# Performance work log

Measured on AMD Instinct MI355X. Metric: run time of the kernel, lower is better.

## Reference

```python
import jax, jax.numpy as jnp
import numpy as np

M, B, U, D = 65536, 128, 256, 512
USAGE_DECAY = 0.95

def _l2n(x, axis):
    # tf.nn.l2_normalize semantics (K.l2_normalize)
    return x / jnp.sqrt(jnp.maximum(jnp.sum(x * x, axis=axis, keepdims=True), 1e-12))

def _lstm_cell(x, h, c, kernel, rec_kernel, bias):
    # Keras LSTMCell: gates in order i, f, c, o
    z = x @ kernel + h @ rec_kernel + bias  # [B, 4U]
    zi, zf, zc, zo = jnp.split(z, 4, axis=-1)
    i = jax.nn.sigmoid(zi)
    f = jax.nn.sigmoid(zf)
    c_new = f * c + i * jnp.tanh(zc)
    o = jax.nn.sigmoid(zo)
    h_new = o * jnp.tanh(c_new)
    return h_new, c_new

def setup_inputs() -> dict:
    key = jax.random.key(0)
    ks = jax.random.split(key, 10)
    return {
        "inputs": jax.random.normal(ks[0], (B, D), jnp.float32),
        "r_tm1": jnp.zeros((B, U), jnp.float32),
        "m_tm1": jax.random.uniform(ks[1], (M, U), jnp.float32),
        "c_wu_tm1": jax.random.uniform(ks[2], (M, B), jnp.float32),
        "c_wlu_tm1": jnp.zeros((M, B), jnp.float32),
        "c_wr_tm1": jax.random.uniform(ks[3], (M, B), jnp.float32),
        "h_tm1": jax.random.normal(ks[4], (B, U), jnp.float32) * 0.1,
        "cc_tm1": jax.random.normal(ks[5], (B, U), jnp.float32) * 0.1,
        "kernel": jax.random.normal(ks[6], (D + U, 4 * U), jnp.float32) * 0.02,
        "rec_kernel": jax.random.normal(ks[7], (U, 4 * U), jnp.float32) * 0.02,
        "bias": jnp.zeros((4 * U,), jnp.float32),
        "write_gate": jax.random.normal(ks[8], (1,), jnp.float32),
    }

def reference(inputs, r_tm1, m_tm1, c_wu_tm1, c_wlu_tm1, c_wr_tm1,
              h_tm1, cc_tm1, kernel, rec_kernel, bias, write_gate):
    # Controller step on [inputs, r_tm1]
    ctrl_in = jnp.concatenate([inputs, r_tm1], axis=1)          # [B, D+U]
    key_list, cc = _lstm_cell(ctrl_in, h_tm1, cc_tm1, kernel, rec_kernel, bias)  # [B, U]

    wg = jax.nn.sigmoid(write_gate)                              # [1]
    # NOTE: faithful to source -- scalar (1 - wg) is ADDED elementwise, then c_wlu added
    c_ww = wg * c_wr_tm1 + (1.0 - wg) + c_wlu_tm1                # [M, B]

    # cosine-similarity addressing
    cos = _l2n(key_list, 1) @ _l2n(m_tm1, 1).T                   # [B, M]
    # K.softmax on the transposed matrix => softmax over the BATCH axis (faithful)
    c_wr = jax.nn.softmax(cos.T, axis=-1)                        # [M, B]
    read = c_wr.T @ m_tm1                                        # [B, U]

    c_wu = USAGE_DECAY * c_wu_tm1 + c_wr + c_ww                  # [M, B]

    # top_k(c_wu.T, M): v.T[-1,:] is the per-batch minimum over slots
    mins = jnp.min(c_wu, axis=0)                                 # [B]
    min_idx = jnp.argmin(c_wu, axis=0)                           # [B]
    b_star = jnp.argmin(mins)                                    # scalar
    i_star = min_idx[b_star]                                     # global least-used slot

    c_wlu = (c_wu <= mins[None, :]).astype(jnp.float32)          # [M, B]

    # zeroing_matrix = one_hot(i_star broadcast to B cols, on=0, off=1) [M,B];
    # dot(zeroing[M,B], ones[B,U]) -> rows = B except zeroed row (faithful B scaling)
    keep = 1.0 - jax.nn.one_hot(i_star, M, dtype=jnp.float32)    # [M]
    memory = (float(B) * keep)[:, None] * m_tm1                  # [M, U]
    memory = c_ww @ key_list + memory                            # [M, U]

    return (read, memory, c_wu, c_wlu, c_wr, key_list, cc)
```

## Files before the change

### kernel.cpp

```cpp
#include <hip/hip_runtime.h>
#include <hip/hip_bf16.h>
#include <math.h>

#define NM 65536
#define NB 128
#define NU 256
#define ND 512

constexpr size_t OUT_READ = 0;
constexpr size_t OUT_MEM  = 32768;
constexpr size_t OUT_CWU  = OUT_MEM + 16777216;
constexpr size_t OUT_CWLU = OUT_CWU + 8388608;
constexpr size_t OUT_CWR  = OUT_CWLU + 8388608;
constexpr size_t OUT_KEY  = OUT_CWR + 8388608;
constexpr size_t OUT_CC   = OUT_KEY + 32768;

constexpr size_t WS_KLNT   = 0;
constexpr size_t WS_MINENC = 131072;
constexpr size_t WS_MINS   = 132096;
constexpr size_t WS_ISTAR  = 132608;
constexpr size_t WS_PART   = 135168;

typedef __attribute__((ext_vector_type(8))) short short8v;
typedef __attribute__((ext_vector_type(4))) float floatx4;

__device__ __forceinline__ unsigned fenc(float x) {
    unsigned u = __float_as_uint(x);
    return (u & 0x80000000u) ? ~u : (u | 0x80000000u);
}
__device__ __forceinline__ float fdec(unsigned e) {
    unsigned u = (e & 0x80000000u) ? (e ^ 0x80000000u) : ~e;
    return __uint_as_float(u);
}
__device__ __forceinline__ float sigm(float x) { return 1.0f / (1.0f + expf(-x)); }
__device__ __forceinline__ unsigned short f2b(float f) {
    __hip_bfloat16 h = __float2bfloat16(f);
    return *reinterpret_cast<unsigned short*>(&h);
}

__global__ __launch_bounds__(256) void k_lstm(
    const float* __restrict__ xin_g, const float* __restrict__ r_tm1,
    const float* __restrict__ h_tm1, const float* __restrict__ cc_tm1,
    const float* __restrict__ Wk, const float* __restrict__ Wr,
    const float* __restrict__ bias, float* __restrict__ out,
    float* __restrict__ klnT, unsigned long long* __restrict__ minenc)
{
    const int b = blockIdx.x, t = threadIdx.x;
    __shared__ float xin[ND + NU];
    __shared__ float hh[NU];
    __shared__ float red[NU];
    for (int k = t; k < ND; k += 256) xin[k] = xin_g[b * ND + k];
    xin[ND + t] = r_tm1[b * NU + t];
    hh[t] = h_tm1[b * NU + t];
    out[OUT_READ + b * NU + t] = 0.f;
    if (b == 0 && t < NB) minenc[t] = ~0ULL;
    __syncthreads();

    float zi = bias[t], zf = bias[NU + t], zc = bias[2 * NU + t], zo = bias[3 * NU + t];
    #pragma unroll 4
    for (int k = 0; k < ND + NU; ++k) {
        const float x = xin[k];
        const float* w = Wk + (size_t)k * (4 * NU);
        zi += x * w[t]; zf += x * w[NU + t]; zc += x * w[2 * NU + t]; zo += x * w[3 * NU + t];
    }
    #pragma unroll 4
    for (int k = 0; k < NU; ++k) {
        const float x = hh[k];
        const float* w = Wr + (size_t)k * (4 * NU);
        zi += x * w[t]; zf += x * w[NU + t]; zc += x * w[2 * NU + t]; zo += x * w[3 * NU + t];
    }
    const float gi = sigm(zi), gf = sigm(zf), gc = tanhf(zc), go = sigm(zo);
    const float cold = cc_tm1[b * NU + t];
    const float cn = __fadd_rn(__fmul_rn(gf, cold), __fmul_rn(gi, gc));
    const float hn = __fmul_rn(go, tanhf(cn));
    out[OUT_KEY + b * NU + t] = hn;
    out[OUT_CC + b * NU + t] = cn;
    red[t] = hn * hn;
    __syncthreads();
    for (int s = 128; s > 0; s >>= 1) { if (t < s) red[t] += red[t + s]; __syncthreads(); }
    const float nrm = sqrtf(fmaxf(red[0], 1e-12f));
    klnT[t * NB + b] = hn / nrm;
}

__global__ __launch_bounds__(256, 2) void k_dot(
    const float* __restrict__ mT, const float* __restrict__ klnT,
    const float* __restrict__ cwr_t, const float* __restrict__ cwlu_t,
    const float* __restrict__ cwu_t, const float* __restrict__ wgp,
    float* __restrict__ out, unsigned long long* __restrict__ minenc)
{
    __shared__ float smem[16384];
    __shared__ float rn_s[128];
    const int t = threadIdx.x, w = t >> 6, l = t & 63;
    const int tx = t & 15, ty = t >> 4;
    const int b0 = tx * 8, s0 = ty * 8;
    const int sb = blockIdx.x * 128;

    #pragma unroll 4
    for (int i = 0; i < 32; ++i) {
        const int s = w * 32 + i;
        const float4 mv = *(const float4*)(mT + (size_t)(sb + s) * NU + l * 4);
        float ss = mv.x * mv.x + mv.y * mv.y + mv.z * mv.z + mv.w * mv.w;
        #pragma unroll
        for (int d = 1; d < 64; d <<= 1) ss += __shfl_xor(ss, d);
        if (l == 0) rn_s[s] = sqrtf(fmaxf(ss, 1e-12f));
    }

    const int sl = t & 127, ug = t >> 7;
    const int ku_ = t >> 4, kb = (t & 15) * 4;

    float acc[8][8];
    #pragma unroll
    for (int i = 0; i < 8; ++i)
        #pragma unroll
        for (int j = 0; j < 8; ++j) acc[i][j] = 0.f;

    float4 gm[2], gk[2];
    #pragma unroll
    for (int i = 0; i < 2; ++i) {
        gm[i] = *(const float4*)(mT + (size_t)(sb + sl) * NU + (ug + 2 * i) * 4);
        gk[i] = *(const float4*)(klnT + (size_t)ku_ * NB + kb + i * 64);
    }
    for (int c = 0; c < 16; ++c) {
        const int mo = (c & 1) * 2048;
        const int ko = 4096 + (c & 1) * 2048;
        #pragma unroll
        for (int i = 0; i < 2; ++i) {
            const int uo = (ug + 2 * i) * 4;
            smem[mo + (uo + 0) * 128 + sl] = gm[i].x;
            smem[mo + (uo + 1) * 128 + sl] = gm[i].y;
            smem[mo + (uo + 2) * 128 + sl] = gm[i].z;
            smem[mo + (uo + 3) * 128 + sl] = gm[i].w;
            *(float4*)&smem[ko + ku_ * 128 + kb + i * 64] = gk[i];
        }
        __syncthreads();
        if (c < 15) {
            const int uc = (c + 1) * 16;
            #pragma unroll
            for (int i = 0; i < 2; ++i) {
                gm[i] = *(const float4*)(mT + (size_t)(sb + sl) * NU + uc + (ug + 2 * i) * 4);
                gk[i] = *(const float4*)(klnT + (size_t)(uc + ku_) * NB + kb + i * 64);
            }
        }
        #pragma unroll 4
        for (int u = 0; u < 16; ++u) {
            const float4 sv0 = *(const float4*)&smem[mo + u * 128 + s0];
            const float4 sv1 = *(const float4*)&smem[mo + u * 128 + s0 + 4];
            const float4 kv0 = *(const float4*)&smem[ko + u * 128 + b0];
            const float4 kv1 = *(const float4*)&smem[ko + u * 128 + b0 + 4];
            const float sv[8] = {sv0.x, sv0.y, sv0.z, sv0.w, sv1.x, sv1.y, sv1.z, sv1.w};
            const float kv[8] = {kv0.x, kv0.y, kv0.z, kv0.w, kv1.x, kv1.y, kv1.z, kv1.w};
            #pragma unroll
            for (int i = 0; i < 8; ++i)
                #pragma unroll
                for (int j = 0; j < 8; ++j)
                    acc[i][j] += sv[i] * kv[j];
        }
        __syncthreads();
    }

    #pragma unroll
    for (int i = 0; i < 8; ++i) {
        *(float4*)&smem[(s0 + i) * 128 + b0]     = make_float4(acc[i][0], acc[i][1], acc[i][2], acc[i][3]);
        *(float4*)&smem[(s0 + i) * 128 + b0 + 4] = make_float4(acc[i][4], acc[i][5], acc[i][6], acc[i][7]);
    }
    __syncthreads();

    const float wg = sigm(wgp[0]);
    const float omw = __fsub_rn(1.f, wg);
    unsigned long long lmin0 = ~0ULL, lmin1 = ~0ULL;
    #pragma unroll 2
    for (int i = 0; i < 32; ++i) {
        const int s = w * 32 + i;
        const int m = sb + s;
        const float2 dv = *(const float2*)&smem[s * 128 + 2 * l];
        const float rnv = rn_s[s];
        const float2 wrt = ((const float2*)(cwr_t + (size_t)m * NB))[l];
        const float2 wlu = ((const float2*)(cwlu_t + (size_t)m * NB))[l];
        const float2 wut = ((const float2*)(cwu_t + (size_t)m * NB))[l];
        const float c0 = dv.x / rnv, c1 = dv.y / rnv;
        float mx = fmaxf(c0, c1);
        #pragma unroll
        for (int d = 1; d < 64; d <<= 1) mx = fmaxf(mx, __shfl_xor(mx, d));
        const float e0 = expf(c0 - mx), e1 = expf(c1 - mx);
        float sm = e0 + e1;
        #pragma unroll
        for (int d = 1; d < 64; d <<= 1) sm += __shfl_xor(sm, d);
        const float w0 = e0 / sm, w1 = e1 / sm;
        const float cww0 = __fadd_rn(__fadd_rn(__fmul_rn(wg, wrt.x), omw), wlu.x);
        const float cww1 = __fadd_rn(__fadd_rn(__fmul_rn(wg, wrt.y), omw), wlu.y);
        const float cu0 = __fadd_rn(__fadd_rn(__fmul_rn(0.95f, wut.x), w0), cww0);
        const float cu1 = __fadd_rn(__fadd_rn(__fmul_rn(0.95f, wut.y), w1), cww1);
        ((float2*)(out + OUT_CWR))[(size_t)m * 64 + l] = make_float2(w0, w1);
        ((float2*)(out + OUT_CWU))[(size_t)m * 64 + l] = make_float2(cu0, cu1);
        const unsigned long long e0u = (((unsigned long long)fenc(cu0)) << 32) | (unsigned)m;
        const unsigned long long e1u = (((unsigned long long)fenc(cu1)) << 32) | (unsigned)m;
        lmin0 = (e0u < lmin0) ? e0u : lmin0;
        lmin1 = (e1u < lmin1) ? e1u : lmin1;
    }
    atomicMin(&minenc[2 * l], lmin0);
    atomicMin(&minenc[2 * l + 1], lmin1);
}

__global__ void k_argmin(const unsigned long long* __restrict__ minenc,
                         float* __restrict__ mins, unsigned* __restrict__ istar)
{
    __shared__ unsigned long long red[NB];
    const int t = threadIdx.x;
    const unsigned long long e = minenc[t];
    const unsigned enc32 = (unsigned)(e >> 32);
    mins[t] = fdec(enc32);
    red[t] = (((unsigned long long)enc32) << 32) | (unsigned)t;
    __syncthreads();
    for (int s = 64; s > 0; s >>= 1) {
        if (t < s) { const unsigned long long o = red[t + s]; if (o < red[t]) red[t] = o; }
        __syncthreads();
    }
    if (t == 0) {
        const unsigned bstar = (unsigned)(red[0] & 0xFFFFFFFFu);
        istar[0] = (unsigned)(minenc[bstar] & 0xFFFFFFFFu);
    }
}

__global__ __launch_bounds__(256, 2) void k_mem(
    const float* __restrict__ mT,
    const float* __restrict__ cwr_t, const float* __restrict__ cwlu_t,
    const float* __restrict__ wgp, const float* __restrict__ mins,
    const unsigned* __restrict__ istar_p, float* __restrict__ out)
{
    __shared__ unsigned short cwwb[128 * 136];
    __shared__ unsigned short keyT[128 * 136];
    const int t = threadIdx.x, w = t >> 6, l = t & 63;
    const int sb = blockIdx.x * 128;
    const float wg = sigm(wgp[0]);
    const float omw = __fsub_rn(1.f, wg);
    const int istar = (int)istar_p[0];

    {
        const int srow = t >> 5;
        const int bc = (t & 31) * 4;
        for (int it = 0; it < 16; ++it) {
            const int s = it * 8 + srow;
            const size_t row = (size_t)(sb + s) * NB + bc;
            const float4 wr = *(const float4*)(cwr_t + row);
            const float4 lu = *(const float4*)(cwlu_t + row);
            const float4 wu = *(const float4*)(out + OUT_CWU + row);
            float4 cw;
            cw.x = __fadd_rn(__fadd_rn(__fmul_rn(wg, wr.x), omw), lu.x);
            cw.y = __fadd_rn(__fadd_rn(__fmul_rn(wg, wr.y), omw), lu.y);
            cw.z = __fadd_rn(__fadd_rn(__fmul_rn(wg, wr.z), omw), lu.z);
            cw.w = __fadd_rn(__fadd_rn(__fmul_rn(wg, wr.w), omw), lu.w);
            ushort4 pk;
            pk.x = f2b(cw.x); pk.y = f2b(cw.y); pk.z = f2b(cw.z); pk.w = f2b(cw.w);
            *(ushort4*)&cwwb[s * 136 + bc] = pk;
            const float4 mb = *(const float4*)(mins + bc);
            float4 wl;
            wl.x = (wu.x <= mb.x) ? 1.f : 0.f;
            wl.y = (wu.y <= mb.y) ? 1.f : 0.f;
            wl.z = (wu.z <= mb.z) ? 1.f : 0.f;
            wl.w = (wu.w <= mb.w) ? 1.f : 0.f;
            *(float4*)(out + OUT_CWLU + row) = wl;
        }
    }

    const int rk = (l >> 4) * 8;
    const int rr = l & 15;

    for (int uh = 0; uh < 2; ++uh) {
        if (uh) __syncthreads();
        {
            const int br = t >> 5;
            const int ko = (t & 31) * 4;
            for (int it = 0; it < 16; ++it) {
                const int b = it * 8 + br;
                const float4 kv = *(const float4*)(out + OUT_KEY + (size_t)b * NU + uh * 128 + ko);
                keyT[(ko + 0) * 136 + b] = f2b(kv.x);
                keyT[(ko + 1) * 136 + b] = f2b(kv.y);
                keyT[(ko + 2) * 136 + b] = f2b(kv.z);
                keyT[(ko + 3) * 136 + b] = f2b(kv.w);
            }
        }
        __syncthreads();

        floatx4 acc0[8], acc1[8];
        #pragma unroll
        for (int ut = 0; ut < 8; ++ut) {
            acc0[ut] = (floatx4){0.f, 0.f, 0.f, 0.f};
            acc1[ut] = (floatx4){0.f, 0.f, 0.f, 0.f};
        }
        #pragma unroll
        for (int kc = 0; kc < 4; ++kc) {
            const short8v a0 = *(const short8v*)&cwwb[(w * 32 + rr) * 136 + kc * 32 + rk];
            const short8v a1 = *(const short8v*)&cwwb[(w * 32 + 16 + rr) * 136 + kc * 32 + rk];
            #pragma unroll
            for (int ut = 0; ut < 8; ++ut) {
                const short8v bf = *(const short8v*)&keyT[(ut * 16 + rr) * 136 + kc * 32 + rk];
                acc0[ut] = __builtin_amdgcn_mfma_f32_16x16x32_bf16(a0, bf, acc0[ut], 0, 0, 0);
                acc1[ut] = __builtin_amdgcn_mfma_f32_16x16x32_bf16(a1, bf, acc1[ut], 0, 0, 0);
            }
        }

        #pragma unroll
        for (int ut = 0; ut < 8; ++ut) {
            const int gcol = uh * 128 + ut * 16 + rr;
            #pragma unroll
            for (int q = 0; q < 4; ++q) {
                const int grow0 = sb + w * 32 + (l >> 4) * 4 + q;
                const int grow1 = grow0 + 16;
                const float mv0 = mT[(size_t)grow0 * NU + gcol];
                const float mv1 = mT[(size_t)grow1 * NU + gcol];
                const float kf0 = (grow0 == istar) ? 0.f : 128.f;
                const float kf1 = (grow1 == istar) ? 0.f : 128.f;
                out[OUT_MEM + (size_t)grow0 * NU + gcol] = acc0[ut][q] + kf0 * mv0;
                out[OUT_MEM + (size_t)grow1 * NU + gcol] = acc1[ut][q] + kf1 * mv1;
            }
        }
    }
}

template <int USE_PART>
__global__ __launch_bounds__(256) void k_read(
    const float* __restrict__ mT, float* __restrict__ out, float* __restrict__ part)
{
    __shared__ float m_ch[2][8][128];
    __shared__ float cwr_ch[2][8][128];
    const int t = threadIdx.x;
    const int r = blockIdx.x, ri = r >> 1, uh = r & 1;
    const int s0 = ri * 256;
    const int b0 = (t & 15) * 8, u0 = (t >> 4) * 8;
    const int ssl = t >> 5, sul = (t & 31) * 4;

    float4 acc[8][2];
    #pragma unroll
    for (int bi = 0; bi < 8; ++bi) { acc[bi][0] = make_float4(0,0,0,0); acc[bi][1] = make_float4(0,0,0,0); }

    float4 pm = *(const float4*)(mT + (size_t)(s0 + ssl) * NU + uh * 128 + sul);
    float4 pc = *(const float4*)(out + OUT_CWR + (size_t)(s0 + ssl) * NB + sul);

    for (int c = 0; c < 32; ++c) {
        const int buf = c & 1;
        *(float4*)&m_ch[buf][ssl][sul] = pm;
        *(float4*)&cwr_ch[buf][ssl][sul] = pc;
        __syncthreads();
        if (c + 1 < 32) {
            const size_t sn = (size_t)(s0 + (c + 1) * 8 + ssl);
            pm = *(const float4*)(mT + sn * NU + uh * 128 + sul);
            pc = *(const float4*)(out + OUT_CWR + sn * NB + sul);
        }
        #pragma unroll
        for (int sj = 0; sj < 8; ++sj) {
            const float4 ca = *(const float4*)&cwr_ch[buf][sj][b0];
            const float4 cb = *(const float4*)&cwr_ch[buf][sj][b0 + 4];
            const float4 ma = *(const float4*)&m_ch[buf][sj][u0];
            const float4 mb = *(const float4*)&m_ch[buf][sj][u0 + 4];
            const float cwa[8] = {ca.x, ca.y, ca.z, ca.w, cb.x, cb.y, cb.z, cb.w};
            #pragma unroll
            for (int bi = 0; bi < 8; ++bi) {
                acc[bi][0].x += cwa[bi] * ma.x; acc[bi][0].y += cwa[bi] * ma.y;
                acc[bi][0].z += cwa[bi] * ma.z; acc[bi][0].w += cwa[bi] * ma.w;
                acc[bi][1].x += cwa[bi] * mb.x; acc[bi][1].y += cwa[bi] * mb.y;
                acc[bi][1].z += cwa[bi] * mb.z; acc[bi][1].w += cwa[bi] * mb.w;
            }
        }
    }

    if (USE_PART) {
        float* dst = part + (size_t)r * (128 * 128);
        #pragma unroll
        for (int bi = 0; bi < 8; ++bi) {
            *(float4*)(dst + (size_t)(b0 + bi) * 128 + u0) = acc[bi][0];
            *(float4*)(dst + (size_t)(b0 + bi) * 128 + u0 + 4) = acc[bi][1];
        }
    } else {
        #pragma unroll
        for (int bi = 0; bi < 8; ++bi) {
            const float v[8] = {acc[bi][0].x, acc[bi][0].y, acc[bi][0].z, acc[bi][0].w,
                                acc[bi][1].x, acc[bi][1].y, acc[bi][1].z, acc[bi][1].w};
            #pragma unroll
            for (int q = 0; q < 8; ++q)
                atomicAdd(out + OUT_READ + (size_t)(b0 + bi) * NU + uh * 128 + u0 + q, v[q]);
        }
    }
}

__global__ __launch_bounds__(256) void k_redread(const float* __restrict__ part,
                                                 float* __restrict__ out)
{
    const int b = blockIdx.x, u = threadIdx.x;
    const int uh = u >> 7, ul = u & 127;
    float s = 0.f;
    #pragma unroll 4
    for (int ri = 0; ri < 256; ++ri)
        s += part[((size_t)(ri * 2 + uh) * 128 + b) * 128 + ul];
    out[OUT_READ + b * NU + u] = s;
}

extern "C" void kernel_launch(void* const* d_in, const int* in_sizes, int n_in,
                              void* d_out, int out_size, void* d_ws, size_t ws_size,
                              hipStream_t stream)
{
    const float* inputs    = (const float*)d_in[0];
    const float* r_tm1     = (const float*)d_in[1];
    const float* m_tm1     = (const float*)d_in[2];
    const float* c_wu_tm1  = (const float*)d_in[3];
    const float* c_wlu_tm1 = (const float*)d_in[4];
    const float* c_wr_tm1  = (const float*)d_in[5];
    const float* h_tm1     = (const float*)d_in[6];
    const float* cc_tm1    = (const float*)d_in[7];
    const float* Wk        = (const float*)d_in[8];
    const float* Wr        = (const float*)d_in[9];
    const float* bias      = (const float*)d_in[10];
    const float* wgate     = (const float*)d_in[11];
    float* out = (float*)d_out;
    char* ws = (char*)d_ws;

    float* klnT = (float*)(ws + WS_KLNT);
    unsigned long long* minenc = (unsigned long long*)(ws + WS_MINENC);
    float* mins = (float*)(ws + WS_MINS);
    unsigned* istar = (unsigned*)(ws + WS_ISTAR);
    float* part = (float*)(ws + WS_PART);
    const bool use_part = ws_size >= WS_PART + (size_t)512 * 128 * 128 * 4;

    hipLaunchKernelGGL(k_lstm, dim3(128), dim3(256), 0, stream,
                       inputs, r_tm1, h_tm1, cc_tm1, Wk, Wr, bias, out, klnT, minenc);
    hipLaunchKernelGGL(k_dot, dim3(512), dim3(256), 0, stream,
                       m_tm1, klnT, c_wr_tm1, c_wlu_tm1, c_wu_tm1, wgate, out, minenc);
    hipLaunchKernelGGL(k_argmin, dim3(1), dim3(128), 0, stream, minenc, mins, istar);
    hipLaunchKernelGGL(k_mem, dim3(512), dim3(256), 0, stream,
                       m_tm1, c_wr_tm1, c_wlu_tm1, wgate, mins, istar, out);
    if (use_part) {
        hipLaunchKernelGGL((k_read<1>), dim3(512), dim3(256), 0, stream, m_tm1, out, part);
        hipLaunchKernelGGL(k_redread, dim3(128), dim3(256), 0, stream, part, out);
    } else {
        hipLaunchKernelGGL((k_read<0>), dim3(512), dim3(256), 0, stream, m_tm1, out, part);
    }
}
```

Measured before the change: 423.5 us.

## Halve k_dot LDS footprint and deepen register prefetch to raise occupancy

Shrinks the k_dot shared buffer from 64KB to 32KB by writing the accumulator tile back in two 64-slot halves for the softmax/usage epilogue, and raises launch bounds from 2 to 4 blocks per CU. The global loads for the GEMM are prefetched two chunks ahead into alternating register sets (A/B), and LDS stores for the next chunk happen after compute so only one barrier per iteration is needed. The aim is more resident waves to hide memory latency. The cost is higher register pressure (extra prefetch registers plus an 8x8 accumulator) under a tighter launch bound, which may cause spills, plus an extra barrier in the epilogue.

```diff
diff --git a/kernel.cpp b/kernel.cpp
--- a/kernel.cpp
+++ b/kernel.cpp
@@ -82,18 +82,29 @@
     klnT[t * NB + b] = hn / nrm;
 }
 
-__global__ __launch_bounds__(256, 2) void k_dot(
+__global__ __launch_bounds__(256, 4) void k_dot(
     const float* __restrict__ mT, const float* __restrict__ klnT,
     const float* __restrict__ cwr_t, const float* __restrict__ cwlu_t,
     const float* __restrict__ cwu_t, const float* __restrict__ wgp,
     float* __restrict__ out, unsigned long long* __restrict__ minenc)
 {
-    __shared__ float smem[16384];
+    __shared__ float smem[8192];
     __shared__ float rn_s[128];
     const int t = threadIdx.x, w = t >> 6, l = t & 63;
     const int tx = t & 15, ty = t >> 4;
     const int b0 = tx * 8, s0 = ty * 8;
     const int sb = blockIdx.x * 128;
+    const int sl = t & 127, ug = t >> 7;
+    const int ku_ = t >> 4, kb = (t & 15) * 4;
+
+    float4 gmA[2], gkA[2], gmB[2], gkB[2];
+    #pragma unroll
+    for (int i = 0; i < 2; ++i) {
+        gmA[i] = *(const float4*)(mT + (size_t)(sb + sl) * NU + (ug + 2 * i) * 4);
+        gkA[i] = *(const float4*)(klnT + (size_t)ku_ * NB + kb + i * 64);
+        gmB[i] = *(const float4*)(mT + (size_t)(sb + sl) * NU + 16 + (ug + 2 * i) * 4);
+        gkB[i] = *(const float4*)(klnT + (size_t)(16 + ku_) * NB + kb + i * 64);
+    }
 
     #pragma unroll 4
     for (int i = 0; i < 32; ++i) {
@@ -105,8 +116,15 @@
         if (l == 0) rn_s[s] = sqrtf(fmaxf(ss, 1e-12f));
     }
 
-    const int sl = t & 127, ug = t >> 7;
-    const int ku_ = t >> 4, kb = (t & 15) * 4;
+    #pragma unroll
+    for (int i = 0; i < 2; ++i) {
+        const int uo = (ug + 2 * i) * 4;
+        smem[uo * 128 + sl]       = gmA[i].x;
+        smem[(uo + 1) * 128 + sl] = gmA[i].y;
+        smem[(uo + 2) * 128 + sl] = gmA[i].z;
+        smem[(uo + 3) * 128 + sl] = gmA[i].w;
+        *(float4*)&smem[4096 + ku_ * 128 + kb + i * 64] = gkA[i];
+    }
 
     float acc[8][8];
     #pragma unroll
@@ -114,33 +132,26 @@
         #pragma unroll
         for (int j = 0; j < 8; ++j) acc[i][j] = 0.f;
 
-    float4 gm[2], gk[2];
-    #pragma unroll
-    for (int i = 0; i < 2; ++i) {
-        gm[i] = *(const float4*)(mT + (size_t)(sb + sl) * NU + (ug + 2 * i) * 4);
-        gk[i] = *(const float4*)(klnT + (size_t)ku_ * NB + kb + i * 64);
-    }
     for (int c = 0; c < 16; ++c) {
+        __syncthreads();
+        if (c < 14) {
+            const int uc = (c + 2) * 16;
+            if ((c & 1) == 0) {
+                #pragma unroll
+                for (int i = 0; i < 2; ++i) {
+                    gmA[i] = *(const float4*)(mT + (size_t)(sb + sl) * NU + uc + (ug + 2 * i) * 4);
+                    gkA[i] = *(const float4*)(klnT + (size_t)(uc + ku_) * NB + kb + i * 64);
+                }
+            } else {
+                #pragma unroll
+                for (int i = 0; i < 2; ++i) {
+                    gmB[i] = *(const float4*)(mT + (size_t)(sb + sl) * NU + uc + (ug + 2 * i) * 4);
+                    gkB[i] = *(const float4*)(klnT + (size_t)(uc + ku_) * NB + kb + i * 64);
+                }
+            }
+        }
         const int mo = (c & 1) * 2048;
         const int ko = 4096 + (c & 1) * 2048;
-        #pragma unroll
-        for (int i = 0; i < 2; ++i) {
-            const int uo = (ug + 2 * i) * 4;
-            smem[mo + (uo + 0) * 128 + sl] = gm[i].x;
-            smem[mo + (uo + 1) * 128 + sl] = gm[i].y;
-            smem[mo + (uo + 2) * 128 + sl] = gm[i].z;
-            smem[mo + (uo + 3) * 128 + sl] = gm[i].w;
-            *(float4*)&smem[ko + ku_ * 128 + kb + i * 64] = gk[i];
-        }
-        __syncthreads();
-        if (c < 15) {
-            const int uc = (c + 1) * 16;
-            #pragma unroll
-            for (int i = 0; i < 2; ++i) {
-                gm[i] = *(const float4*)(mT + (size_t)(sb + sl) * NU + uc + (ug + 2 * i) * 4);
-                gk[i] = *(const float4*)(klnT + (size_t)(uc + ku_) * NB + kb + i * 64);
-            }
-        }
         #pragma unroll 4
         for (int u = 0; u < 16; ++u) {
             const float4 sv0 = *(const float4*)&smem[mo + u * 128 + s0];
@@ -155,47 +166,78 @@
                 for (int j = 0; j < 8; ++j)
                     acc[i][j] += sv[i] * kv[j];
         }
-        __syncthreads();
-    }
-
-    #pragma unroll
-    for (int i = 0; i < 8; ++i) {
-        *(float4*)&smem[(s0 + i) * 128 + b0]     = make_float4(acc[i][0], acc[i][1], acc[i][2], acc[i][3]);
-        *(float4*)&smem[(s0 + i) * 128 + b0 + 4] = make_float4(acc[i][4], acc[i][5], acc[i][6], acc[i][7]);
-    }
-    __syncthreads();
+        if (c < 15) {
+            const int mo1 = ((c + 1) & 1) * 2048;
+            const int ko1 = 4096 + ((c + 1) & 1) * 2048;
+            if ((c & 1) == 0) {
+                #pragma unroll
+                for (int i = 0; i < 2; ++i) {
+                    const int uo = (ug + 2 * i) * 4;
+                    smem[mo1 + uo * 128 + sl]       = gmB[i].x;
+                    smem[mo1 + (uo + 1) * 128 + sl] = gmB[i].y;
+                    smem[mo1 + (uo + 2) * 128 + sl] = gmB[i].z;
+                    smem[mo1 + (uo + 3) * 128 + sl] = gmB[i].w;
+                    *(float4*)&smem[ko1 + ku_ * 128 + kb + i * 64] = gkB[i];
+                }
+            } else {
+                #pragma unroll
+                for (int i = 0; i < 2; ++i) {
+                    const int uo = (ug + 2 * i) * 4;
+                    smem[mo1 + uo * 128 + sl]       = gmA[i].x;
+                    smem[mo1 + (uo + 1) * 128 + sl] = gmA[i].y;
+                    smem[mo1 + (uo + 2) * 128 + sl] = gmA[i].z;
+                    smem[mo1 + (uo + 3) * 128 + sl] = gmA[i].w;
+                    *(float4*)&smem[ko1 + ku_ * 128 + kb + i * 64] = gkA[i];
+                }
+            }
+        }
+    }
 
     const float wg = sigm(wgp[0]);
     const float omw = __fsub_rn(1.f, wg);
     unsigned long long lmin0 = ~0ULL, lmin1 = ~0ULL;
-    #pragma unroll 2
-    for (int i = 0; i < 32; ++i) {
-        const int s = w * 32 + i;
-        const int m = sb + s;
-        const float2 dv = *(const float2*)&smem[s * 128 + 2 * l];
-        const float rnv = rn_s[s];
-        const float2 wrt = ((const float2*)(cwr_t + (size_t)m * NB))[l];
-        const float2 wlu = ((const float2*)(cwlu_t + (size_t)m * NB))[l];
-        const float2 wut = ((const float2*)(cwu_t + (size_t)m * NB))[l];
-        const float c0 = dv.x / rnv, c1 = dv.y / rnv;
-        float mx = fmaxf(c0, c1);
-        #pragma unroll
-        for (int d = 1; d < 64; d <<= 1) mx = fmaxf(mx, __shfl_xor(mx, d));
-        const float e0 = expf(c0 - mx), e1 = expf(c1 - mx);
-        float sm = e0 + e1;
-        #pragma unroll
-        for (int d = 1; d < 64; d <<= 1) sm += __shfl_xor(sm, d);
-        const float w0 = e0 / sm, w1 = e1 / sm;
-        const float cww0 = __fadd_rn(__fadd_rn(__fmul_rn(wg, wrt.x), omw), wlu.x);
-        const float cww1 = __fadd_rn(__fadd_rn(__fmul_rn(wg, wrt.y), omw), wlu.y);
-        const float cu0 = __fadd_rn(__fadd_rn(__fmul_rn(0.95f, wut.x), w0), cww0);
-        const float cu1 = __fadd_rn(__fadd_rn(__fmul_rn(0.95f, wut.y), w1), cww1);
-        ((float2*)(out + OUT_CWR))[(size_t)m * 64 + l] = make_float2(w0, w1);
-        ((float2*)(out + OUT_CWU))[(size_t)m * 64 + l] = make_float2(cu0, cu1);
-        const unsigned long long e0u = (((unsigned long long)fenc(cu0)) << 32) | (unsigned)m;
-        const unsigned long long e1u = (((unsigned long long)fenc(cu1)) << 32) | (unsigned)m;
-        lmin0 = (e0u < lmin0) ? e0u : lmin0;
-        lmin1 = (e1u < lmin1) ? e1u : lmin1;
+    #pragma unroll
+    for (int h = 0; h < 2; ++h) {
+        __syncthreads();
+        if ((ty >> 3) == h) {
+            const int ls0 = s0 & 63;
+            #pragma unroll
+            for (int i = 0; i < 8; ++i) {
+                *(float4*)&smem[(ls0 + i) * 128 + b0]     = make_float4(acc[i][0], acc[i][1], acc[i][2], acc[i][3]);
+                *(float4*)&smem[(ls0 + i) * 128 + b0 + 4] = make_float4(acc[i][4], acc[i][5], acc[i][6], acc[i][7]);
+            }
+        }
+        __syncthreads();
+        #pragma unroll 2
+        for (int i = 0; i < 16; ++i) {
+            const int ls = w * 16 + i;
+            const int s = h * 64 + ls;
+            const int m = sb + s;
+            const float2 dv = *(const float2*)&smem[ls * 128 + 2 * l];
+            const float rnv = rn_s[s];
+            const float2 wrt = ((const float2*)(cwr_t + (size_t)m * NB))[l];
+            const float2 wlu = ((const float2*)(cwlu_t + (size_t)m * NB))[l];
+            const float2 wut = ((const float2*)(cwu_t + (size_t)m * NB))[l];
+            const float c0 = dv.x / rnv, c1 = dv.y / rnv;
+            float mx = fmaxf(c0, c1);
+            #pragma unroll
+            for (int d = 1; d < 64; d <<= 1) mx = fmaxf(mx, __shfl_xor(mx, d));
+            const float e0 = expf(c0 - mx), e1 = expf(c1 - mx);
+            float sm = e0 + e1;
+            #pragma unroll
+            for (int d = 1; d < 64; d <<= 1) sm += __shfl_xor(sm, d);
+            const float w0 = e0 / sm, w1 = e1 / sm;
+            const float cww0 = __fadd_rn(__fadd_rn(__fmul_rn(wg, wrt.x), omw), wlu.x);
+            const float cww1 = __fadd_rn(__fadd_rn(__fmul_rn(wg, wrt.y), omw), wlu.y);
+            const float cu0 = __fadd_rn(__fadd_rn(__fmul_rn(0.95f, wut.x), w0), cww0);
+            const float cu1 = __fadd_rn(__fadd_rn(__fmul_rn(0.95f, wut.y), w1), cww1);
+            ((float2*)(out + OUT_CWR))[(size_t)m * 64 + l] = make_float2(w0, w1);
+            ((float2*)(out + OUT_CWU))[(size_t)m * 64 + l] = make_float2(cu0, cu1);
+            const unsigned long long e0u = (((unsigned long long)fenc(cu0)) << 32) | (unsigned)m;
+            const unsigned long long e1u = (((unsigned long long)fenc(cu1)) << 32) | (unsigned)m;
+            lmin0 = (e0u < lmin0) ? e0u : lmin0;
+            lmin1 = (e1u < lmin1) ? e1u : lmin1;
+        }
     }
     atomicMin(&minenc[2 * l], lmin0);
     atomicMin(&minenc[2 * l + 1], lmin1);
```

Measured after the change: 445.2 us. 1.05x slower.

## Compute read GEMM with bf16 MFMA instead of FP32 LDS-tiled FMA

Applied to the files above, without the earlier changes.

Replaces the shared-memory double-buffered FP32 outer-product loop in k_read with bf16 MFMA 16x16x32 instructions. Operands are loaded straight from global memory and converted to bf16 per lane, with no LDS staging or barriers. This removes the scalar FMA throughput cost of the c_wr^T @ m product. In exchange it loses precision from the bf16 inputs and uses strided, less coalesced global loads.

```diff
diff --git a/kernel.cpp b/kernel.cpp
--- a/kernel.cpp
+++ b/kernel.cpp
@@ -321,64 +321,58 @@
 __global__ __launch_bounds__(256) void k_read(
     const float* __restrict__ mT, float* __restrict__ out, float* __restrict__ part)
 {
-    __shared__ float m_ch[2][8][128];
-    __shared__ float cwr_ch[2][8][128];
-    const int t = threadIdx.x;
+    const int t = threadIdx.x, w = t >> 6, l = t & 63;
     const int r = blockIdx.x, ri = r >> 1, uh = r & 1;
-    const int s0 = ri * 256;
-    const int b0 = (t & 15) * 8, u0 = (t >> 4) * 8;
-    const int ssl = t >> 5, sul = (t & 31) * 4;
-
-    float4 acc[8][2];
+    const int rk = (l >> 4) * 8, rr = l & 15;
+    const float* cwr = out + OUT_CWR;
+
+    floatx4 acc[2][8];
     #pragma unroll
-    for (int bi = 0; bi < 8; ++bi) { acc[bi][0] = make_float4(0,0,0,0); acc[bi][1] = make_float4(0,0,0,0); }
-
-    float4 pm = *(const float4*)(mT + (size_t)(s0 + ssl) * NU + uh * 128 + sul);
-    float4 pc = *(const float4*)(out + OUT_CWR + (size_t)(s0 + ssl) * NB + sul);
-
-    for (int c = 0; c < 32; ++c) {
-        const int buf = c & 1;
-        *(float4*)&m_ch[buf][ssl][sul] = pm;
-        *(float4*)&cwr_ch[buf][ssl][sul] = pc;
-        __syncthreads();
-        if (c + 1 < 32) {
-            const size_t sn = (size_t)(s0 + (c + 1) * 8 + ssl);
-            pm = *(const float4*)(mT + sn * NU + uh * 128 + sul);
-            pc = *(const float4*)(out + OUT_CWR + sn * NB + sul);
-        }
-        #pragma unroll
-        for (int sj = 0; sj < 8; ++sj) {
-            const float4 ca = *(const float4*)&cwr_ch[buf][sj][b0];
-            const float4 cb = *(const float4*)&cwr_ch[buf][sj][b0 + 4];
-            const float4 ma = *(const float4*)&m_ch[buf][sj][u0];
-            const float4 mb = *(const float4*)&m_ch[buf][sj][u0 + 4];
-            const float cwa[8] = {ca.x, ca.y, ca.z, ca.w, cb.x, cb.y, cb.z, cb.w};
-            #pragma unroll
-            for (int bi = 0; bi < 8; ++bi) {
-                acc[bi][0].x += cwa[bi] * ma.x; acc[bi][0].y += cwa[bi] * ma.y;
-                acc[bi][0].z += cwa[bi] * ma.z; acc[bi][0].w += cwa[bi] * ma.w;
-                acc[bi][1].x += cwa[bi] * mb.x; acc[bi][1].y += cwa[bi] * mb.y;
-                acc[bi][1].z += cwa[bi] * mb.z; acc[bi][1].w += cwa[bi] * mb.w;
-            }
-        }
+    for (int bt = 0; bt < 2; ++bt)
+        #pragma unroll
+        for (int ut = 0; ut < 8; ++ut) acc[bt][ut] = (floatx4){0.f, 0.f, 0.f, 0.f};
+
+    for (int c = 0; c < 8; ++c) {
+        const size_t m0 = (size_t)(ri * 256 + c * 32 + rk);
+        short8v a[2];
+        #pragma unroll
+        for (int bt = 0; bt < 2; ++bt) {
+            const float* ap = cwr + m0 * NB + w * 32 + bt * 16 + rr;
+            #pragma unroll
+            for (int i = 0; i < 8; ++i) a[bt][i] = (short)f2b(ap[i * NB]);
+        }
+        short8v bf[8];
+        #pragma unroll
+        for (int ut = 0; ut < 8; ++ut) {
+            const float* bp = mT + m0 * NU + uh * 128 + ut * 16 + rr;
+            #pragma unroll
+            for (int i = 0; i < 8; ++i) bf[ut][i] = (short)f2b(bp[i * NU]);
+        }
+        #pragma unroll
+        for (int bt = 0; bt < 2; ++bt)
+            #pragma unroll
+            for (int ut = 0; ut < 8; ++ut)
+                acc[bt][ut] = __builtin_amdgcn_mfma_f32_16x16x32_bf16(a[bt], bf[ut], acc[bt][ut], 0, 0, 0);
     }
 
     if (USE_PART) {
         float* dst = part + (size_t)r * (128 * 128);
         #pragma unroll
-        for (int bi = 0; bi < 8; ++bi) {
-            *(float4*)(dst + (size_t)(b0 + bi) * 128 + u0) = acc[bi][0];
-            *(float4*)(dst + (size_t)(b0 + bi) * 128 + u0 + 4) = acc[bi][1];
-        }
+        for (int bt = 0; bt < 2; ++bt)
+            #pragma unroll
+            for (int ut = 0; ut < 8; ++ut)
+                #pragma unroll
+                for (int q = 0; q < 4; ++q)
+                    dst[(size_t)(w * 32 + bt * 16 + (l >> 4) * 4 + q) * 128 + ut * 16 + rr] = acc[bt][ut][q];
     } else {
         #pragma unroll
-        for (int bi = 0; bi < 8; ++bi) {
-            const float v[8] = {acc[bi][0].x, acc[bi][0].y, acc[bi][0].z, acc[bi][0].w,
-                                acc[bi][1].x, acc[bi][1].y, acc[bi][1].z, acc[bi][1].w};
-            #pragma unroll
-            for (int q = 0; q < 8; ++q)
-                atomicAdd(out + OUT_READ + (size_t)(b0 + bi) * NU + uh * 128 + u0 + q, v[q]);
-        }
+        for (int bt = 0; bt < 2; ++bt)
+            #pragma unroll
+            for (int ut = 0; ut < 8; ++ut)
+                #pragma unroll
+                for (int q = 0; q < 4; ++q)
+                    atomicAdd(out + OUT_READ + (size_t)(w * 32 + bt * 16 + (l >> 4) * 4 + q) * NU
+                                  + uh * 128 + ut * 16 + rr, acc[bt][ut][q]);
     }
 }
 
```

After: 405.0 us. 4.4% less time.
